# Kernel tuning notes

Measured on AMD Instinct MI355X. Metric: run time of the kernel, lower is better.

The kernel has to match this reference:

```python
import jax, jax.numpy as jnp
import numpy as np

S, H, HEADS = 2048, 1024, 16   # seq_len, hidden_size, num attention heads
E, NM, P = 256, 1024, 2048     # num entities, total mentions, num candidate pairs
PH = 1024                      # pair_hidden_size


def setup_inputs() -> dict:
    key = jax.random.key(0)
    ks = jax.random.split(key, 13)
    s = 1.0 / np.sqrt(H)
    return {
        "sequence_output": jax.random.normal(ks[0], (S, H), jnp.float32),
        "attention": jax.random.uniform(ks[1], (HEADS, S, S), jnp.float32),
        "mention_idx": jax.random.randint(ks[2], (NM,), 0, S, jnp.int32),
        "entity_ids": jnp.sort(jax.random.randint(ks[3], (NM,), 0, E, jnp.int32)),
        "pair_h": jax.random.randint(ks[4], (P,), 0, E, jnp.int32),
        "pair_t": jax.random.randint(ks[5], (P,), 0, E, jnp.int32),
        "W_head": jax.random.normal(ks[6], (H, PH), jnp.float32) * s,
        "b_head": jnp.zeros((PH,), jnp.float32),
        "W_tail": jax.random.normal(ks[7], (H, PH), jnp.float32) * s,
        "b_tail": jnp.zeros((PH,), jnp.float32),
        "W_ctx": jax.random.normal(ks[8], (H, PH), jnp.float32) * s,
        "W_bil": jax.random.normal(ks[9], (PH, PH), jnp.float32) * s,
        "b_bil": jnp.zeros((), jnp.float32),
    }


def reference(sequence_output, attention, mention_idx, entity_ids, pair_h, pair_t,
              W_head, b_head, W_tail, b_tail, W_ctx, W_bil, b_bil):
    # ---- entity aggregation: ragged segment logsumexp (embs) + segment mean (atts) ----
    vals = sequence_output[mention_idx]                               # [NM, H]
    counts = jax.ops.segment_sum(jnp.ones((NM,), vals.dtype), entity_ids, num_segments=E)
    has = counts > 0                                                  # [E]
    seg_max = jax.ops.segment_max(vals, entity_ids, num_segments=E)   # [E, H]
    seg_max = jnp.where(has[:, None], seg_max, 0.0)
    sums = jax.ops.segment_sum(jnp.exp(vals - seg_max[entity_ids]), entity_ids, num_segments=E)
    ent_emb = jnp.where(has[:, None],
                        seg_max + jnp.log(jnp.where(has[:, None], sums, 1.0)),
                        0.0)                                          # [E, H]
    m_att = jnp.transpose(attention[:, mention_idx, :], (1, 0, 2))    # [NM, HEADS, S]
    ent_att = jax.ops.segment_sum(m_att, entity_ids, num_segments=E)
    ent_att = ent_att / jnp.maximum(counts, 1.0)[:, None, None]       # [E, HEADS, S]

    # ---- pair scoring ----
    hs, ts = ent_emb[pair_h], ent_emb[pair_t]                         # [P, H]
    pair_att = (ent_att[pair_h] * ent_att[pair_t]).sum(axis=1)        # [P, S]
    pair_att = pair_att / (pair_att.sum(axis=-1, keepdims=True) + 1e-6)
    contexts = pair_att @ sequence_output                             # [P, H]
    ctx_p = contexts @ W_ctx                                          # [P, PH]
    z_s = jnp.tanh(hs @ W_head + b_head + ctx_p)
    z_o = jnp.tanh(ts @ W_tail + b_tail + ctx_p)
    logits = jnp.einsum('pi,ij,pj->p', z_s, W_bil, z_o) + b_bil       # [P]
    return logits
```

## Files before the change

### kernel.cpp

```cpp
#include <hip/hip_runtime.h>
#include <hip/hip_bf16.h>
#include <math.h>
#include <stdint.h>

#define S_LEN  2048
#define HID    1024
#define NHEADS 16
#define NE     256
#define NMEN   1024
#define NP     2048
#define PHID   1024

typedef __attribute__((ext_vector_type(8))) short bf16x8;
typedef __attribute__((ext_vector_type(4))) float f32x4;
typedef unsigned int uint;

__device__ inline void seg_bounds(const int* __restrict__ entity_ids, int e,
                                  int& start, int& end) {
    int lo = 0, hi = NMEN;
    while (lo < hi) { int mid = (lo + hi) >> 1; if (entity_ids[mid] < e) lo = mid + 1; else hi = mid; }
    start = lo;
    hi = NMEN;
    while (lo < hi) { int mid = (lo + hi) >> 1; if (entity_ids[mid] <= e) lo = mid + 1; else hi = mid; }
    end = lo;
}

__device__ __forceinline__ void load_lds16(const void* g, void* l) {
    __builtin_amdgcn_global_load_lds(
        (const __attribute__((address_space(1))) uint32_t*)g,
        (__attribute__((address_space(3))) uint32_t*)l,
        16, 0, 0);
}

__device__ __forceinline__ float bflo(uint u) { return __uint_as_float(u << 16); }
__device__ __forceinline__ float bfhi(uint u) { return __uint_as_float(u & 0xffff0000u); }
__device__ __forceinline__ uint pk2(float a, float b) {
    __hip_bfloat16 ha = __float2bfloat16(a), hb = __float2bfloat16(b);
    unsigned short ua = *(unsigned short*)&ha, ub = *(unsigned short*)&hb;
    return (uint)ua | ((uint)ub << 16);
}

__global__ void prep_ent_kernel(const float* __restrict__ seq,
                                const float* __restrict__ attention,
                                const float* __restrict__ w0, const float* __restrict__ w1,
                                const float* __restrict__ w2, const float* __restrict__ wbil,
                                const int* __restrict__ mention_idx,
                                const int* __restrict__ entity_ids,
                                __hip_bfloat16* __restrict__ seqB,
                                __hip_bfloat16* __restrict__ o0, __hip_bfloat16* __restrict__ o1,
                                __hip_bfloat16* __restrict__ o2, __hip_bfloat16* __restrict__ obil,
                                uint2* __restrict__ eaB,
                                __hip_bfloat16* __restrict__ ent_emb)
{
    __shared__ float tbuf[32][33];
    __shared__ int sb[2];
    int id = blockIdx.x;
    if (id < 1024) {
        long i = (long)id * 256 + threadIdx.x;
        const float4* in4 = (const float4*)seq;
        float4 a = in4[2 * i], b = in4[2 * i + 1];
        uint4 o;
        o.x = pk2(a.x, a.y); o.y = pk2(a.z, a.w);
        o.z = pk2(b.x, b.y); o.w = pk2(b.z, b.w);
        ((uint4*)seqB)[i] = o;
        return;
    }
    if (id < 4096) {
        int t = id - 1024;
        int z = t >> 10;
        const float* in = (z == 0) ? w0 : (z == 1) ? w1 : w2;
        __hip_bfloat16* out = (z == 0) ? o0 : (z == 1) ? o1 : o2;
        int r0 = ((t >> 5) & 31) * 32, c0 = (t & 31) * 32;
        int j = threadIdx.x & 31, i0 = threadIdx.x >> 5;
        for (int i = i0; i < 32; i += 8)
            tbuf[i][j] = in[(long)(r0 + i) * 1024 + c0 + j];
        __syncthreads();
        for (int i = i0; i < 32; i += 8)
            out[(long)(c0 + i) * 1024 + r0 + j] = __float2bfloat16(tbuf[j][i]);
        return;
    }
    if (id < 4608) {
        long i = (long)(id - 4096) * 256 + threadIdx.x;
        const float4* in4 = (const float4*)wbil;
        float4 a = in4[2 * i], b = in4[2 * i + 1];
        uint4 o;
        o.x = pk2(a.x, a.y); o.y = pk2(a.z, a.w);
        o.z = pk2(b.x, b.y); o.w = pk2(b.z, b.w);
        ((uint4*)obil)[i] = o;
        return;
    }
    int t = id - 4608;
    int e = t & 255, role = t >> 8;
    if (threadIdx.x == 0) { int s, tt; seg_bounds(entity_ids, e, s, tt); sb[0] = s; sb[1] = tt; }
    __syncthreads();
    int start = sb[0], end = sb[1];

    if (role < 16) {
        const float4* att4 = (const float4*)attention;
        int h = role;
        float inv = 1.f / fmaxf((float)(end - start), 1.f);
        for (int s4 = threadIdx.x; s4 < S_LEN / 4; s4 += 256) {
            float ax = 0.f, ay = 0.f, az = 0.f, aw = 0.f;
            for (int i = start; i < end; ++i) {
                float4 v = att4[((long)h * S_LEN + mention_idx[i]) * (S_LEN / 4) + s4];
                ax += v.x; ay += v.y; az += v.z; aw += v.w;
            }
            uint2 o; o.x = pk2(ax * inv, ay * inv); o.y = pk2(az * inv, aw * inv);
            eaB[((long)e * NHEADS + h) * (S_LEN / 4) + s4] = o;
        }
    } else {
        const float4* seq4 = (const float4*)seq;
        int col4 = threadIdx.x;
        uint2 o;
        if (end <= start) {
            o.x = 0; o.y = 0;
            ((uint2*)ent_emb)[(long)e * 256 + col4] = o;
            return;
        }
        float mx = -INFINITY, my = -INFINITY, mz = -INFINITY, mw = -INFINITY;
        for (int i = start; i < end; ++i) {
            float4 v = seq4[(long)mention_idx[i] * 256 + col4];
            mx = fmaxf(mx, v.x); my = fmaxf(my, v.y); mz = fmaxf(mz, v.z); mw = fmaxf(mw, v.w);
        }
        float sx = 0.f, sy = 0.f, sz = 0.f, sw = 0.f;
        for (int i = start; i < end; ++i) {
            float4 v = seq4[(long)mention_idx[i] * 256 + col4];
            sx += expf(v.x - mx); sy += expf(v.y - my); sz += expf(v.z - mz); sw += expf(v.w - mw);
        }
        o.x = pk2(mx + logf(sx), my + logf(sy));
        o.y = pk2(mz + logf(sz), mw + logf(sw));
        ((uint2*)ent_emb)[(long)e * 256 + col4] = o;
    }
}

template <int MODE>
__device__ __forceinline__ void gemm_epilogue(
    f32x4 (&acc)[4][4], void* __restrict__ Cout,
    const __hip_bfloat16* __restrict__ zvec, float* __restrict__ out,
    int M, int N, int bm, int bn, int bz, int wr, int wc, int lane)
{
    int lr = lane & 15;
    int q4 = (lane >> 4) * 4;
    if (MODE == 0) {
#pragma unroll
        for (int fm = 0; fm < 4; ++fm)
#pragma unroll
            for (int fn = 0; fn < 4; ++fn) {
                int row = bm + wr * 64 + fm * 16 + q4;
                int col = bn + wc * 64 + fn * 16 + lr;
#pragma unroll
                for (int r = 0; r < 4; ++r)
                    ((float*)Cout)[((long)bz * M + row + r) * N + col] = acc[fm][fn][r];
            }
    } else if (MODE == 1) {
#pragma unroll
        for (int fm = 0; fm < 4; ++fm)
#pragma unroll
            for (int fn = 0; fn < 4; ++fn) {
                int row = bm + wr * 64 + fm * 16 + q4;
                int col = bn + wc * 64 + fn * 16 + lr;
#pragma unroll
                for (int r = 0; r < 4; ++r)
                    ((__hip_bfloat16*)Cout)[(long)(row + r) * N + col] = __float2bfloat16(acc[fm][fn][r]);
            }
    } else if (MODE == 3) {
#pragma unroll
        for (int fm = 0; fm < 4; ++fm)
#pragma unroll
            for (int fn = 0; fn < 4; ++fn) {
                int row = bm + wr * 64 + fm * 16 + q4;
                int col = bn + wc * 64 + fn * 16 + lr;
#pragma unroll
                for (int r = 0; r < 4; ++r)
                    ((__hip_bfloat16*)Cout)[((long)bz * M + row + r) * N + col] = __float2bfloat16(acc[fm][fn][r]);
            }
    } else {
#pragma unroll
        for (int fm = 0; fm < 4; ++fm) {
#pragma unroll
            for (int r = 0; r < 4; ++r) {
                int row = bm + wr * 64 + fm * 16 + q4 + r;
                float v = 0.f;
#pragma unroll
                for (int fn = 0; fn < 4; ++fn) {
                    int col = bn + wc * 64 + fn * 16 + lr;
                    v += acc[fm][fn][r] * __bfloat162float(zvec[(long)row * N + col]);
                }
                v += __shfl_xor(v, 1, 64);
                v += __shfl_xor(v, 2, 64);
                v += __shfl_xor(v, 4, 64);
                v += __shfl_xor(v, 8, 64);
                if (lr == 0) atomicAdd(out + row, v);
            }
        }
    }
}

template <int MODE>
__device__ __forceinline__ void gemm_core(
    const __hip_bfloat16* __restrict__ A,
    const __hip_bfloat16* __restrict__ Bt,
    void* __restrict__ Cout, const __hip_bfloat16* __restrict__ zvec, float* __restrict__ out,
    int M, int N, int Kstride, int kLen,
    int bx, int by, int bz,
    short (*As)[128][8], short (*Bs)[128][8])
{
    int tid = threadIdx.x;
    int lane = tid & 63, wid = tid >> 6;
    int wr = wid >> 1, wc = wid & 1;
    int bm = by * 128, bn = bx * 128;
    int kBeg = bz * kLen;

    const __hip_bfloat16* gsrc[8];
    void* ldst[8];
#pragma unroll
    for (int i = 0; i < 8; ++i) {
        int c = wid * 8 + i;
        int isA = (c < 16) ? 1 : 0;
        int cc = isA ? c : c - 16;
        int kg2 = cc >> 1, rh = cc & 1;
        gsrc[i] = (isA ? A + (long)(bm + rh * 64 + lane) * Kstride
                       : Bt + (long)(bn + rh * 64 + lane) * Kstride) + kBeg + kg2 * 8;
        ldst[i] = isA ? (void*)&As[kg2][rh * 64][0] : (void*)&Bs[kg2][rh * 64][0];
    }

    f32x4 acc[4][4] = {};
    int kg = lane >> 4, lr = lane & 15;

    for (int k0 = 0; k0 < kLen; k0 += 64) {
#pragma unroll
        for (int i = 0; i < 8; ++i)
            load_lds16(gsrc[i] + k0, ldst[i]);
        __syncthreads();
#pragma unroll
        for (int sub = 0; sub < 2; ++sub) {
            bf16x8 af[4], bfr[4];
#pragma unroll
            for (int f = 0; f < 4; ++f) {
                af[f]  = *(const bf16x8*)&As[sub * 4 + kg][wr * 64 + f * 16 + lr][0];
                bfr[f] = *(const bf16x8*)&Bs[sub * 4 + kg][wc * 64 + f * 16 + lr][0];
            }
#pragma unroll
            for (int fm = 0; fm < 4; ++fm)
#pragma unroll
                for (int fn = 0; fn < 4; ++fn)
                    acc[fm][fn] = __builtin_amdgcn_mfma_f32_16x16x32_bf16(af[fm], bfr[fn], acc[fm][fn], 0, 0, 0);
        }
        __syncthreads();
    }
    gemm_epilogue<MODE>(acc, Cout, zvec, out, M, N, bm, bn, bz, wr, wc, lane);
}

template <int MODE>
__device__ __forceinline__ void gemm_core_db(
    const __hip_bfloat16* __restrict__ A,
    const __hip_bfloat16* __restrict__ Bt,
    void* __restrict__ Cout, const __hip_bfloat16* __restrict__ zvec, float* __restrict__ out,
    int M, int N, int Kstride, int kLen,
    int bx, int by, int bz,
    short (*As)[8][128][8], short (*Bs)[8][128][8])
{
    int tid = threadIdx.x;
    int lane = tid & 63, wid = tid >> 6;
    int wr = wid >> 1, wc = wid & 1;
    int bm = by * 128, bn = bx * 128;
    int kBeg = bz * kLen;

    const __hip_bfloat16* gsrc[8];
    void *ld0[8], *ld1[8];
#pragma unroll
    for (int i = 0; i < 8; ++i) {
        int c = wid * 8 + i;
        int isA = (c < 16) ? 1 : 0;
        int cc = isA ? c : c - 16;
        int kg2 = cc >> 1, rh = cc & 1;
        gsrc[i] = (isA ? A + (long)(bm + rh * 64 + lane) * Kstride
                       : Bt + (long)(bn + rh * 64 + lane) * Kstride) + kBeg + kg2 * 8;
        ld0[i] = isA ? (void*)&As[0][kg2][rh * 64][0] : (void*)&Bs[0][kg2][rh * 64][0];
        ld1[i] = isA ? (void*)&As[1][kg2][rh * 64][0] : (void*)&Bs[1][kg2][rh * 64][0];
    }

    f32x4 acc[4][4] = {};
    int kg = lane >> 4, lr = lane & 15;
    int nSteps = kLen >> 6;

#define STAGE_DB(t, ld) { _Pragma("unroll") \
    for (int i = 0; i < 8; ++i) load_lds16(gsrc[i] + (t) * 64, ld[i]); }
#define COMPUTE_DB(AsB, BsB) { _Pragma("unroll") \
    for (int sub = 0; sub < 2; ++sub) { \
        bf16x8 af[4], bfr[4]; \
        _Pragma("unroll") for (int f = 0; f < 4; ++f) { \
            af[f]  = *(const bf16x8*)&AsB[sub * 4 + kg][wr * 64 + f * 16 + lr][0]; \
            bfr[f] = *(const bf16x8*)&BsB[sub * 4 + kg][wc * 64 + f * 16 + lr][0]; \
        } \
        _Pragma("unroll") for (int fm = 0; fm < 4; ++fm) \
        _Pragma("unroll") for (int fn = 0; fn < 4; ++fn) \
            acc[fm][fn] = __builtin_amdgcn_mfma_f32_16x16x32_bf16(af[fm], bfr[fn], acc[fm][fn], 0, 0, 0); \
    } }

    STAGE_DB(0, ld0);
    __syncthreads();
    for (int step = 0; step < nSteps; step += 2) {
        STAGE_DB(step + 1, ld1);
        COMPUTE_DB(As[0], Bs[0]);
        __syncthreads();
        if (step + 2 < nSteps) STAGE_DB(step + 2, ld0);
        COMPUTE_DB(As[1], Bs[1]);
        __syncthreads();
    }
#undef STAGE_DB
#undef COMPUTE_DB
    gemm_epilogue<MODE>(acc, Cout, zvec, out, M, N, bm, bn, bz, wr, wc, lane);
}

__launch_bounds__(256)
__global__ void pair_seqw_ehet(const __hip_bfloat16* __restrict__ WctxT,
                               const __hip_bfloat16* __restrict__ seqB,
                               __hip_bfloat16* __restrict__ seqWT,
                               const __hip_bfloat16* __restrict__ embB,
                               const __hip_bfloat16* __restrict__ WhtT,
                               float* __restrict__ ehetP,
                               const uint4* __restrict__ ea,
                               const int* __restrict__ pair_h,
                               const int* __restrict__ pair_t,
                               uint4* __restrict__ patt)
{
    __shared__ short As[8][128][8];
    __shared__ short Bs[8][128][8];
    int id = blockIdx.x;
    if (id < 128) {
        gemm_core<1>(WctxT, seqB, seqWT, nullptr, nullptr,
                     PHID, S_LEN, HID, HID, id & 15, id >> 4, 0, As, Bs);
        return;
    }
    if (id < 256) {
        int u = id - 128;
        gemm_core<0>(embB, WhtT, ehetP, nullptr, nullptr,
                     NE, 2 * PHID, HID, HID / 4, u & 15, (u >> 4) & 1, u >> 5, As, Bs);
        return;
    }
    __shared__ float wsum[4];
    int p = id - 256;
    long bh = (long)pair_h[p] * NHEADS * (S_LEN / 8);
    long bt = (long)pair_t[p] * NHEADS * (S_LEN / 8);
    int s8 = threadIdx.x;
    float a0 = 0, a1 = 0, a2 = 0, a3 = 0, a4 = 0, a5 = 0, a6 = 0, a7 = 0;
#pragma unroll
    for (int h = 0; h < NHEADS; ++h) {
        uint4 xa = ea[bh + h * (S_LEN / 8) + s8];
        uint4 xb = ea[bt + h * (S_LEN / 8) + s8];
        a0 += bflo(xa.x) * bflo(xb.x); a1 += bfhi(xa.x) * bfhi(xb.x);
        a2 += bflo(xa.y) * bflo(xb.y); a3 += bfhi(xa.y) * bfhi(xb.y);
        a4 += bflo(xa.z) * bflo(xb.z); a5 += bfhi(xa.z) * bfhi(xb.z);
        a6 += bflo(xa.w) * bflo(xb.w); a7 += bfhi(xa.w) * bfhi(xb.w);
    }
    float psum = a0 + a1 + a2 + a3 + a4 + a5 + a6 + a7;
#pragma unroll
    for (int off = 32; off > 0; off >>= 1)
        psum += __shfl_down(psum, off, 64);
    int lane = threadIdx.x & 63, wid = threadIdx.x >> 6;
    if (lane == 0) wsum[wid] = psum;
    __syncthreads();
    float inv = 1.f / (wsum[0] + wsum[1] + wsum[2] + wsum[3] + 1e-6f);
    uint4 o;
    o.x = pk2(a0 * inv, a1 * inv); o.y = pk2(a2 * inv, a3 * inv);
    o.z = pk2(a4 * inv, a5 * inv); o.w = pk2(a6 * inv, a7 * inv);
    patt[(long)p * (S_LEN / 8) + s8] = o;
}

__launch_bounds__(256)
__global__ void gemm_ctxp_reduce(const __hip_bfloat16* __restrict__ pattB,
                                 const __hip_bfloat16* __restrict__ seqWT,
                                 __hip_bfloat16* __restrict__ ctxpB,
                                 const float* __restrict__ ehetP,
                                 float* __restrict__ ehet)
{
    __shared__ short As[2][8][128][8];
    __shared__ short Bs[2][8][128][8];
    int id = blockIdx.x;
    if (id < 512) {
        int f = (id & 7) * 64 + (id >> 3);
        int bx = f >> 6, inner = f & 63;
        int by = inner & 15, bz = inner >> 4;
        gemm_core_db<3>(pattB, seqWT, ctxpB, nullptr, nullptr,
                        NP, PHID, S_LEN, S_LEN / 4, bx, by, bz, As, Bs);
        return;
    }
    long i = (long)(id - 512) * 2048 + (long)threadIdx.x * 8;
    const long n = (long)NE * 2 * PHID;
    float4 s0 = make_float4(0.f, 0.f, 0.f, 0.f), s1 = s0;
#pragma unroll
    for (int s = 0; s < 4; ++s) {
        float4 a = *(const float4*)&ehetP[s * n + i];
        float4 b = *(const float4*)&ehetP[s * n + i + 4];
        s0.x += a.x; s0.y += a.y; s0.z += a.z; s0.w += a.w;
        s1.x += b.x; s1.y += b.y; s1.z += b.z; s1.w += b.w;
    }
    *(float4*)&ehet[i] = s0;
    *(float4*)&ehet[i + 4] = s1;
}

__global__ void zs_zo_kernel(const __hip_bfloat16* __restrict__ ctxpB,
                             const float* __restrict__ ehet,
                             const float* __restrict__ b_head,
                             const float* __restrict__ b_tail,
                             const int* __restrict__ pair_h,
                             const int* __restrict__ pair_t,
                             __hip_bfloat16* __restrict__ zs,
                             __hip_bfloat16* __restrict__ zo,
                             const float* __restrict__ b_bil, float* __restrict__ out)
{
    long base = ((long)blockIdx.x * 256 + threadIdx.x) * 4;
    if (base < NP) {
        float bb = b_bil[0];
#pragma unroll
        for (int i = 0; i < 4; ++i) out[base + i] = bb;
    }
    int p = (int)(base >> 10);
    int j = (int)(base & (PHID - 1));
    const long n = (long)NP * PHID;
    float c0 = 0.f, c1 = 0.f, c2 = 0.f, c3 = 0.f;
#pragma unroll
    for (int s = 0; s < 4; ++s) {
        uint2 u = *(const uint2*)&ctxpB[s * n + base];
        c0 += bflo(u.x); c1 += bfhi(u.x); c2 += bflo(u.y); c3 += bfhi(u.y);
    }
    float4 eh = *(const float4*)&ehet[(long)pair_h[p] * 2048 + j];
    float4 et = *(const float4*)&ehet[(long)pair_t[p] * 2048 + 1024 + j];
    float4 bh = *(const float4*)&b_head[j];
    float4 bt = *(const float4*)&b_tail[j];
    float h0 = tanhf(eh.x + bh.x + c0), h1 = tanhf(eh.y + bh.y + c1);
    float h2 = tanhf(eh.z + bh.z + c2), h3 = tanhf(eh.w + bh.w + c3);
    float t0 = tanhf(et.x + bt.x + c0), t1 = tanhf(et.y + bt.y + c1);
    float t2 = tanhf(et.z + bt.z + c2), t3 = tanhf(et.w + bt.w + c3);
    uint2 ozs; ozs.x = pk2(h0, h1); ozs.y = pk2(h2, h3);
    uint2 ozo; ozo.x = pk2(t0, t1); ozo.y = pk2(t2, t3);
    *(uint2*)&zs[base] = ozs;
    *(uint2*)&zo[base] = ozo;
}

template <int MODE>
__launch_bounds__(256)
__global__ void gemm_single_db(const __hip_bfloat16* __restrict__ A,
                               const __hip_bfloat16* __restrict__ Bt,
                               void* __restrict__ Cout,
                               const __hip_bfloat16* __restrict__ zvec,
                               float* __restrict__ out,
                               int M, int N, int Kstride, int kLen)
{
    __shared__ short As[2][8][128][8];
    __shared__ short Bs[2][8][128][8];
    gemm_core_db<MODE>(A, Bt, Cout, zvec, out, M, N, Kstride, kLen,
                       blockIdx.x, blockIdx.y, blockIdx.z, As, Bs);
}

extern "C" void kernel_launch(void* const* d_in, const int* in_sizes, int n_in,
                              void* d_out, int out_size, void* d_ws, size_t ws_size,
                              hipStream_t stream)
{
    const float* seq        = (const float*)d_in[0];
    const float* attention  = (const float*)d_in[1];
    const int*   mention_idx= (const int*)  d_in[2];
    const int*   entity_ids = (const int*)  d_in[3];
    const int*   pair_h     = (const int*)  d_in[4];
    const int*   pair_t     = (const int*)  d_in[5];
    const float* W_head     = (const float*)d_in[6];
    const float* b_head     = (const float*)d_in[7];
    const float* W_tail     = (const float*)d_in[8];
    const float* b_tail     = (const float*)d_in[9];
    const float* W_ctx      = (const float*)d_in[10];
    const float* W_bil      = (const float*)d_in[11];
    const float* b_bil      = (const float*)d_in[12];
    float* out = (float*)d_out;

    char* w = (char*)d_ws;
    __hip_bfloat16* seqB  = (__hip_bfloat16*)(w + 0);
    __hip_bfloat16* WctxT = (__hip_bfloat16*)(w + (4l << 20));
    __hip_bfloat16* WhtT  = (__hip_bfloat16*)(w + (6l << 20));
    __hip_bfloat16* WbilB = (__hip_bfloat16*)(w + (10l << 20));
    __hip_bfloat16* embB  = (__hip_bfloat16*)(w + (12l << 20));
    __hip_bfloat16* eaB   = (__hip_bfloat16*)(w + (13l << 20));
    __hip_bfloat16* pattB = (__hip_bfloat16*)(w + (29l << 20));
    __hip_bfloat16* seqWT = (__hip_bfloat16*)(w + (37l << 20));
    __hip_bfloat16* zsB   = (__hip_bfloat16*)(w + (41l << 20));
    __hip_bfloat16* zoB   = (__hip_bfloat16*)(w + (45l << 20));
    __hip_bfloat16* ctxpB = (__hip_bfloat16*)(w + (49l << 20));
    float* ehetP = (float*)(w + (65l << 20));
    float* ehet  = (float*)(w + (73l << 20));

    prep_ent_kernel<<<8960, 256, 0, stream>>>(seq, attention, W_ctx, W_head, W_tail, W_bil,
                                              mention_idx, entity_ids,
                                              seqB, WctxT, WhtT, WhtT + (long)PHID * HID, WbilB,
                                              (uint2*)eaB, embB);

    pair_seqw_ehet<<<2304, 256, 0, stream>>>(WctxT, seqB, seqWT, embB, WhtT, ehetP,
                                             (const uint4*)eaB, pair_h, pair_t, (uint4*)pattB);

    gemm_ctxp_reduce<<<768, 256, 0, stream>>>(pattB, seqWT, ctxpB, ehetP, ehet);

    zs_zo_kernel<<<2048, 256, 0, stream>>>(ctxpB, ehet, b_head, b_tail, pair_h, pair_t,
                                           zsB, zoB, b_bil, out);

    gemm_single_db<2><<<dim3(8, 16, 4), 256, 0, stream>>>(zoB, WbilB, nullptr, zsB, out,
                                                          NP, PHID, HID, HID / 4);
}
```

Measured before the change: 136.6 us.

## Reschedule stages: fuse seq bf16 cast into GEMM, move attention aggregation later

Drops the separate seq fp32-to-bf16 conversion pass. The seq×Wctx GEMM now loads fp32 B tiles directly and converts them to bf16 on the fly while filling LDS. The attention-mean aggregation moves from the first kernel into the second, running concurrently with the small GEMMs. The ehet partial reduction moves into the pair-attention kernel so the ctxp GEMM runs alone. The goal is better load balance across the launch sequence and less workspace traffic, at the cost of a non-async fp32 load path in one GEMM.

```diff
diff --git a/kernel.cpp b/kernel.cpp
--- a/kernel.cpp
+++ b/kernel.cpp
@@ -40,37 +40,24 @@
     return (uint)ua | ((uint)ub << 16);
 }
 
-__global__ void prep_ent_kernel(const float* __restrict__ seq,
-                                const float* __restrict__ attention,
-                                const float* __restrict__ w0, const float* __restrict__ w1,
-                                const float* __restrict__ w2, const float* __restrict__ wbil,
-                                const int* __restrict__ mention_idx,
-                                const int* __restrict__ entity_ids,
-                                __hip_bfloat16* __restrict__ seqB,
-                                __hip_bfloat16* __restrict__ o0, __hip_bfloat16* __restrict__ o1,
-                                __hip_bfloat16* __restrict__ o2, __hip_bfloat16* __restrict__ obil,
-                                uint2* __restrict__ eaB,
-                                __hip_bfloat16* __restrict__ ent_emb)
+__global__ void l0_kernel(const float* __restrict__ seq,
+                          const float* __restrict__ w0, const float* __restrict__ w1,
+                          const float* __restrict__ w2, const float* __restrict__ wbil,
+                          const int* __restrict__ mention_idx,
+                          const int* __restrict__ entity_ids,
+                          __hip_bfloat16* __restrict__ o0, __hip_bfloat16* __restrict__ o1,
+                          __hip_bfloat16* __restrict__ o2, __hip_bfloat16* __restrict__ obil,
+                          __hip_bfloat16* __restrict__ ent_emb)
 {
     __shared__ float tbuf[32][33];
     __shared__ int sb[2];
     int id = blockIdx.x;
-    if (id < 1024) {
-        long i = (long)id * 256 + threadIdx.x;
-        const float4* in4 = (const float4*)seq;
-        float4 a = in4[2 * i], b = in4[2 * i + 1];
-        uint4 o;
-        o.x = pk2(a.x, a.y); o.y = pk2(a.z, a.w);
-        o.z = pk2(b.x, b.y); o.w = pk2(b.z, b.w);
-        ((uint4*)seqB)[i] = o;
-        return;
-    }
-    if (id < 4096) {
-        int t = id - 1024;
-        int z = t >> 10;
+    if (id < 3072) {
+        int z = id >> 10;
         const float* in = (z == 0) ? w0 : (z == 1) ? w1 : w2;
         __hip_bfloat16* out = (z == 0) ? o0 : (z == 1) ? o1 : o2;
-        int r0 = ((t >> 5) & 31) * 32, c0 = (t & 31) * 32;
+        int t = id & 1023;
+        int r0 = (t >> 5) * 32, c0 = (t & 31) * 32;
         int j = threadIdx.x & 31, i0 = threadIdx.x >> 5;
         for (int i = i0; i < 32; i += 8)
             tbuf[i][j] = in[(long)(r0 + i) * 1024 + c0 + j];
@@ -79,8 +66,8 @@
             out[(long)(c0 + i) * 1024 + r0 + j] = __float2bfloat16(tbuf[j][i]);
         return;
     }
-    if (id < 4608) {
-        long i = (long)(id - 4096) * 256 + threadIdx.x;
+    if (id < 3584) {
+        long i = (long)(id - 3072) * 256 + threadIdx.x;
         const float4* in4 = (const float4*)wbil;
         float4 a = in4[2 * i], b = in4[2 * i + 1];
         uint4 o;
@@ -89,48 +76,31 @@
         ((uint4*)obil)[i] = o;
         return;
     }
-    int t = id - 4608;
-    int e = t & 255, role = t >> 8;
+    int e = id - 3584;
     if (threadIdx.x == 0) { int s, tt; seg_bounds(entity_ids, e, s, tt); sb[0] = s; sb[1] = tt; }
     __syncthreads();
     int start = sb[0], end = sb[1];
-
-    if (role < 16) {
-        const float4* att4 = (const float4*)attention;
-        int h = role;
-        float inv = 1.f / fmaxf((float)(end - start), 1.f);
-        for (int s4 = threadIdx.x; s4 < S_LEN / 4; s4 += 256) {
-            float ax = 0.f, ay = 0.f, az = 0.f, aw = 0.f;
-            for (int i = start; i < end; ++i) {
-                float4 v = att4[((long)h * S_LEN + mention_idx[i]) * (S_LEN / 4) + s4];
-                ax += v.x; ay += v.y; az += v.z; aw += v.w;
-            }
-            uint2 o; o.x = pk2(ax * inv, ay * inv); o.y = pk2(az * inv, aw * inv);
-            eaB[((long)e * NHEADS + h) * (S_LEN / 4) + s4] = o;
-        }
-    } else {
-        const float4* seq4 = (const float4*)seq;
-        int col4 = threadIdx.x;
-        uint2 o;
-        if (end <= start) {
-            o.x = 0; o.y = 0;
-            ((uint2*)ent_emb)[(long)e * 256 + col4] = o;
-            return;
-        }
-        float mx = -INFINITY, my = -INFINITY, mz = -INFINITY, mw = -INFINITY;
-        for (int i = start; i < end; ++i) {
-            float4 v = seq4[(long)mention_idx[i] * 256 + col4];
-            mx = fmaxf(mx, v.x); my = fmaxf(my, v.y); mz = fmaxf(mz, v.z); mw = fmaxf(mw, v.w);
-        }
-        float sx = 0.f, sy = 0.f, sz = 0.f, sw = 0.f;
-        for (int i = start; i < end; ++i) {
-            float4 v = seq4[(long)mention_idx[i] * 256 + col4];
-            sx += expf(v.x - mx); sy += expf(v.y - my); sz += expf(v.z - mz); sw += expf(v.w - mw);
-        }
-        o.x = pk2(mx + logf(sx), my + logf(sy));
-        o.y = pk2(mz + logf(sz), mw + logf(sw));
+    const float4* seq4 = (const float4*)seq;
+    int col4 = threadIdx.x;
+    uint2 o;
+    if (end <= start) {
+        o.x = 0; o.y = 0;
         ((uint2*)ent_emb)[(long)e * 256 + col4] = o;
-    }
+        return;
+    }
+    float mx = -INFINITY, my = -INFINITY, mz = -INFINITY, mw = -INFINITY;
+    for (int i = start; i < end; ++i) {
+        float4 v = seq4[(long)mention_idx[i] * 256 + col4];
+        mx = fmaxf(mx, v.x); my = fmaxf(my, v.y); mz = fmaxf(mz, v.z); mw = fmaxf(mw, v.w);
+    }
+    float sx = 0.f, sy = 0.f, sz = 0.f, sw = 0.f;
+    for (int i = start; i < end; ++i) {
+        float4 v = seq4[(long)mention_idx[i] * 256 + col4];
+        sx += expf(v.x - mx); sy += expf(v.y - my); sz += expf(v.z - mz); sw += expf(v.w - mw);
+    }
+    o.x = pk2(mx + logf(sx), my + logf(sy));
+    o.y = pk2(mz + logf(sz), mw + logf(sw));
+    ((uint2*)ent_emb)[(long)e * 256 + col4] = o;
 }
 
 template <int MODE>
@@ -196,97 +166,7 @@
     }
 }
 
-template <int MODE>
-__device__ __forceinline__ void gemm_core(
-    const __hip_bfloat16* __restrict__ A,
-    const __hip_bfloat16* __restrict__ Bt,
-    void* __restrict__ Cout, const __hip_bfloat16* __restrict__ zvec, float* __restrict__ out,
-    int M, int N, int Kstride, int kLen,
-    int bx, int by, int bz,
-    short (*As)[128][8], short (*Bs)[128][8])
-{
-    int tid = threadIdx.x;
-    int lane = tid & 63, wid = tid >> 6;
-    int wr = wid >> 1, wc = wid & 1;
-    int bm = by * 128, bn = bx * 128;
-    int kBeg = bz * kLen;
-
-    const __hip_bfloat16* gsrc[8];
-    void* ldst[8];
-#pragma unroll
-    for (int i = 0; i < 8; ++i) {
-        int c = wid * 8 + i;
-        int isA = (c < 16) ? 1 : 0;
-        int cc = isA ? c : c - 16;
-        int kg2 = cc >> 1, rh = cc & 1;
-        gsrc[i] = (isA ? A + (long)(bm + rh * 64 + lane) * Kstride
-                       : Bt + (long)(bn + rh * 64 + lane) * Kstride) + kBeg + kg2 * 8;
-        ldst[i] = isA ? (void*)&As[kg2][rh * 64][0] : (void*)&Bs[kg2][rh * 64][0];
-    }
-
-    f32x4 acc[4][4] = {};
-    int kg = lane >> 4, lr = lane & 15;
-
-    for (int k0 = 0; k0 < kLen; k0 += 64) {
-#pragma unroll
-        for (int i = 0; i < 8; ++i)
-            load_lds16(gsrc[i] + k0, ldst[i]);
-        __syncthreads();
-#pragma unroll
-        for (int sub = 0; sub < 2; ++sub) {
-            bf16x8 af[4], bfr[4];
-#pragma unroll
-            for (int f = 0; f < 4; ++f) {
-                af[f]  = *(const bf16x8*)&As[sub * 4 + kg][wr * 64 + f * 16 + lr][0];
-                bfr[f] = *(const bf16x8*)&Bs[sub * 4 + kg][wc * 64 + f * 16 + lr][0];
-            }
-#pragma unroll
-            for (int fm = 0; fm < 4; ++fm)
-#pragma unroll
-                for (int fn = 0; fn < 4; ++fn)
-                    acc[fm][fn] = __builtin_amdgcn_mfma_f32_16x16x32_bf16(af[fm], bfr[fn], acc[fm][fn], 0, 0, 0);
-        }
-        __syncthreads();
-    }
-    gemm_epilogue<MODE>(acc, Cout, zvec, out, M, N, bm, bn, bz, wr, wc, lane);
-}
-
-template <int MODE>
-__device__ __forceinline__ void gemm_core_db(
-    const __hip_bfloat16* __restrict__ A,
-    const __hip_bfloat16* __restrict__ Bt,
-    void* __restrict__ Cout, const __hip_bfloat16* __restrict__ zvec, float* __restrict__ out,
-    int M, int N, int Kstride, int kLen,
-    int bx, int by, int bz,
-    short (*As)[8][128][8], short (*Bs)[8][128][8])
-{
-    int tid = threadIdx.x;
-    int lane = tid & 63, wid = tid >> 6;
-    int wr = wid >> 1, wc = wid & 1;
-    int bm = by * 128, bn = bx * 128;
-    int kBeg = bz * kLen;
-
-    const __hip_bfloat16* gsrc[8];
-    void *ld0[8], *ld1[8];
-#pragma unroll
-    for (int i = 0; i < 8; ++i) {
-        int c = wid * 8 + i;
-        int isA = (c < 16) ? 1 : 0;
-        int cc = isA ? c : c - 16;
-        int kg2 = cc >> 1, rh = cc & 1;
-        gsrc[i] = (isA ? A + (long)(bm + rh * 64 + lane) * Kstride
-                       : Bt + (long)(bn + rh * 64 + lane) * Kstride) + kBeg + kg2 * 8;
-        ld0[i] = isA ? (void*)&As[0][kg2][rh * 64][0] : (void*)&Bs[0][kg2][rh * 64][0];
-        ld1[i] = isA ? (void*)&As[1][kg2][rh * 64][0] : (void*)&Bs[1][kg2][rh * 64][0];
-    }
-
-    f32x4 acc[4][4] = {};
-    int kg = lane >> 4, lr = lane & 15;
-    int nSteps = kLen >> 6;
-
-#define STAGE_DB(t, ld) { _Pragma("unroll") \
-    for (int i = 0; i < 8; ++i) load_lds16(gsrc[i] + (t) * 64, ld[i]); }
-#define COMPUTE_DB(AsB, BsB) { _Pragma("unroll") \
+#define COMPUTE_TILE(AsB, BsB) { _Pragma("unroll") \
     for (int sub = 0; sub < 2; ++sub) { \
         bf16x8 af[4], bfr[4]; \
         _Pragma("unroll") for (int f = 0; f < 4; ++f) { \
@@ -298,39 +178,177 @@
             acc[fm][fn] = __builtin_amdgcn_mfma_f32_16x16x32_bf16(af[fm], bfr[fn], acc[fm][fn], 0, 0, 0); \
     } }
 
+template <int MODE>
+__device__ __forceinline__ void gemm_core(
+    const __hip_bfloat16* __restrict__ A,
+    const __hip_bfloat16* __restrict__ Bt,
+    void* __restrict__ Cout, const __hip_bfloat16* __restrict__ zvec, float* __restrict__ out,
+    int M, int N, int Kstride, int kLen,
+    int bx, int by, int bz,
+    short (*As)[128][8], short (*Bs)[128][8])
+{
+    int tid = threadIdx.x;
+    int lane = tid & 63, wid = tid >> 6;
+    int wr = wid >> 1, wc = wid & 1;
+    int bm = by * 128, bn = bx * 128;
+    int kBeg = bz * kLen;
+
+    const __hip_bfloat16* gsrc[8];
+    void* ldst[8];
+#pragma unroll
+    for (int i = 0; i < 8; ++i) {
+        int c = wid * 8 + i;
+        int isA = (c < 16) ? 1 : 0;
+        int cc = isA ? c : c - 16;
+        int kg2 = cc >> 1, rh = cc & 1;
+        gsrc[i] = (isA ? A + (long)(bm + rh * 64 + lane) * Kstride
+                       : Bt + (long)(bn + rh * 64 + lane) * Kstride) + kBeg + kg2 * 8;
+        ldst[i] = isA ? (void*)&As[kg2][rh * 64][0] : (void*)&Bs[kg2][rh * 64][0];
+    }
+
+    f32x4 acc[4][4] = {};
+    int kg = lane >> 4, lr = lane & 15;
+
+    for (int k0 = 0; k0 < kLen; k0 += 64) {
+#pragma unroll
+        for (int i = 0; i < 8; ++i)
+            load_lds16(gsrc[i] + k0, ldst[i]);
+        __syncthreads();
+        COMPUTE_TILE(As, Bs);
+        __syncthreads();
+    }
+    gemm_epilogue<MODE>(acc, Cout, zvec, out, M, N, bm, bn, bz, wr, wc, lane);
+}
+
+__device__ __forceinline__ void gemm_core_f32b(
+    const __hip_bfloat16* __restrict__ A,
+    const float* __restrict__ Bf,
+    __hip_bfloat16* __restrict__ Cout,
+    int M, int N, int Kstride, int kLen,
+    int bx, int by,
+    short (*As)[128][8], short (*Bs)[128][8])
+{
+    int tid = threadIdx.x;
+    int lane = tid & 63, wid = tid >> 6;
+    int wr = wid >> 1, wc = wid & 1;
+    int bm = by * 128, bn = bx * 128;
+
+    const __hip_bfloat16* gA[8];
+    const float* gB[8];
+    void* ldA[8];
+    void* ldB[8];
+#pragma unroll
+    for (int i = 0; i < 8; ++i) {
+        int c = wid * 8 + i;
+        if (c < 16) {
+            int kg2 = c >> 1, rh = c & 1;
+            gA[i] = A + (long)(bm + rh * 64 + lane) * Kstride + kg2 * 8;
+            ldA[i] = (void*)&As[kg2][rh * 64][0];
+            gB[i] = nullptr; ldB[i] = nullptr;
+        } else {
+            int cc = c - 16;
+            int kg2 = cc >> 1, rh = cc & 1;
+            gB[i] = Bf + (long)(bn + rh * 64 + lane) * Kstride + kg2 * 8;
+            ldB[i] = (void*)&Bs[kg2][rh * 64 + lane][0];
+            gA[i] = nullptr; ldA[i] = nullptr;
+        }
+    }
+
+    f32x4 acc[4][4] = {};
+    int kg = lane >> 4, lr = lane & 15;
+
+    for (int k0 = 0; k0 < kLen; k0 += 64) {
+        if (wid < 2) {
+#pragma unroll
+            for (int i = 0; i < 8; ++i)
+                load_lds16(gA[i] + k0, ldA[i]);
+        } else {
+#pragma unroll
+            for (int i = 0; i < 8; ++i) {
+                const float* p = gB[i] + k0;
+                float4 x = *(const float4*)p;
+                float4 y = *(const float4*)(p + 4);
+                uint4 v;
+                v.x = pk2(x.x, x.y); v.y = pk2(x.z, x.w);
+                v.z = pk2(y.x, y.y); v.w = pk2(y.z, y.w);
+                *(uint4*)ldB[i] = v;
+            }
+        }
+        __syncthreads();
+        COMPUTE_TILE(As, Bs);
+        __syncthreads();
+    }
+    gemm_epilogue<1>(acc, (void*)Cout, nullptr, nullptr, M, N, bm, bn, 0, wr, wc, lane);
+}
+
+template <int MODE>
+__device__ __forceinline__ void gemm_core_db(
+    const __hip_bfloat16* __restrict__ A,
+    const __hip_bfloat16* __restrict__ Bt,
+    void* __restrict__ Cout, const __hip_bfloat16* __restrict__ zvec, float* __restrict__ out,
+    int M, int N, int Kstride, int kLen,
+    int bx, int by, int bz,
+    short (*As)[8][128][8], short (*Bs)[8][128][8])
+{
+    int tid = threadIdx.x;
+    int lane = tid & 63, wid = tid >> 6;
+    int wr = wid >> 1, wc = wid & 1;
+    int bm = by * 128, bn = bx * 128;
+    int kBeg = bz * kLen;
+
+    const __hip_bfloat16* gsrc[8];
+    void *ld0[8], *ld1[8];
+#pragma unroll
+    for (int i = 0; i < 8; ++i) {
+        int c = wid * 8 + i;
+        int isA = (c < 16) ? 1 : 0;
+        int cc = isA ? c : c - 16;
+        int kg2 = cc >> 1, rh = cc & 1;
+        gsrc[i] = (isA ? A + (long)(bm + rh * 64 + lane) * Kstride
+                       : Bt + (long)(bn + rh * 64 + lane) * Kstride) + kBeg + kg2 * 8;
+        ld0[i] = isA ? (void*)&As[0][kg2][rh * 64][0] : (void*)&Bs[0][kg2][rh * 64][0];
+        ld1[i] = isA ? (void*)&As[1][kg2][rh * 64][0] : (void*)&Bs[1][kg2][rh * 64][0];
+    }
+
+    f32x4 acc[4][4] = {};
+    int kg = lane >> 4, lr = lane & 15;
+    int nSteps = kLen >> 6;
+
+#define STAGE_DB(t, ld) { _Pragma("unroll") \
+    for (int i = 0; i < 8; ++i) load_lds16(gsrc[i] + (t) * 64, ld[i]); }
+
     STAGE_DB(0, ld0);
     __syncthreads();
     for (int step = 0; step < nSteps; step += 2) {
         STAGE_DB(step + 1, ld1);
-        COMPUTE_DB(As[0], Bs[0]);
+        COMPUTE_TILE(As[0], Bs[0]);
         __syncthreads();
         if (step + 2 < nSteps) STAGE_DB(step + 2, ld0);
-        COMPUTE_DB(As[1], Bs[1]);
+        COMPUTE_TILE(As[1], Bs[1]);
         __syncthreads();
     }
 #undef STAGE_DB
-#undef COMPUTE_DB
     gemm_epilogue<MODE>(acc, Cout, zvec, out, M, N, bm, bn, bz, wr, wc, lane);
 }
 
 __launch_bounds__(256)
-__global__ void pair_seqw_ehet(const __hip_bfloat16* __restrict__ WctxT,
-                               const __hip_bfloat16* __restrict__ seqB,
-                               __hip_bfloat16* __restrict__ seqWT,
-                               const __hip_bfloat16* __restrict__ embB,
-                               const __hip_bfloat16* __restrict__ WhtT,
-                               float* __restrict__ ehetP,
-                               const uint4* __restrict__ ea,
-                               const int* __restrict__ pair_h,
-                               const int* __restrict__ pair_t,
-                               uint4* __restrict__ patt)
+__global__ void l1_kernel(const __hip_bfloat16* __restrict__ WctxT,
+                          const float* __restrict__ seq,
+                          __hip_bfloat16* __restrict__ seqWT,
+                          const __hip_bfloat16* __restrict__ embB,
+                          const __hip_bfloat16* __restrict__ WhtT,
+                          float* __restrict__ ehetP,
+                          const float* __restrict__ attention,
+                          const int* __restrict__ mention_idx,
+                          const int* __restrict__ entity_ids,
+                          uint2* __restrict__ eaB)
 {
     __shared__ short As[8][128][8];
     __shared__ short Bs[8][128][8];
+    __shared__ int sb[2];
     int id = blockIdx.x;
     if (id < 128) {
-        gemm_core<1>(WctxT, seqB, seqWT, nullptr, nullptr,
-                     PHID, S_LEN, HID, HID, id & 15, id >> 4, 0, As, Bs);
+        gemm_core_f32b(WctxT, seq, seqWT, PHID, S_LEN, HID, HID, id & 15, id >> 4, As, Bs);
         return;
     }
     if (id < 256) {
@@ -339,7 +357,48 @@
                      NE, 2 * PHID, HID, HID / 4, u & 15, (u >> 4) & 1, u >> 5, As, Bs);
         return;
     }
+    int t = id - 256;
+    int e = t & 255, h = t >> 8;
+    if (threadIdx.x == 0) { int s, tt; seg_bounds(entity_ids, e, s, tt); sb[0] = s; sb[1] = tt; }
+    __syncthreads();
+    int start = sb[0], end = sb[1];
+    const float4* att4 = (const float4*)attention;
+    float inv = 1.f / fmaxf((float)(end - start), 1.f);
+    for (int s4 = threadIdx.x; s4 < S_LEN / 4; s4 += 256) {
+        float ax = 0.f, ay = 0.f, az = 0.f, aw = 0.f;
+        for (int i = start; i < end; ++i) {
+            float4 v = att4[((long)h * S_LEN + mention_idx[i]) * (S_LEN / 4) + s4];
+            ax += v.x; ay += v.y; az += v.z; aw += v.w;
+        }
+        uint2 o; o.x = pk2(ax * inv, ay * inv); o.y = pk2(az * inv, aw * inv);
+        eaB[((long)e * NHEADS + h) * (S_LEN / 4) + s4] = o;
+    }
+}
+
+__global__ void l2_kernel(const float* __restrict__ ehetP,
+                          float* __restrict__ ehet,
+                          const uint4* __restrict__ ea,
+                          const int* __restrict__ pair_h,
+                          const int* __restrict__ pair_t,
+                          uint4* __restrict__ patt)
+{
     __shared__ float wsum[4];
+    int id = blockIdx.x;
+    if (id < 256) {
+        long i = (long)id * 2048 + (long)threadIdx.x * 8;
+        const long n = (long)NE * 2 * PHID;
+        float4 s0 = make_float4(0.f, 0.f, 0.f, 0.f), s1 = s0;
+#pragma unroll
+        for (int s = 0; s < 4; ++s) {
+            float4 a = *(const float4*)&ehetP[s * n + i];
+            float4 b = *(const float4*)&ehetP[s * n + i + 4];
+            s0.x += a.x; s0.y += a.y; s0.z += a.z; s0.w += a.w;
+            s1.x += b.x; s1.y += b.y; s1.z += b.z; s1.w += b.w;
+        }
+        *(float4*)&ehet[i] = s0;
+        *(float4*)&ehet[i + 4] = s1;
+        return;
+    }
     int p = id - 256;
     long bh = (long)pair_h[p] * NHEADS * (S_LEN / 8);
     long bt = (long)pair_t[p] * NHEADS * (S_LEN / 8);
@@ -369,35 +428,18 @@
 }
 
 __launch_bounds__(256)
-__global__ void gemm_ctxp_reduce(const __hip_bfloat16* __restrict__ pattB,
-                                 const __hip_bfloat16* __restrict__ seqWT,
-                                 __hip_bfloat16* __restrict__ ctxpB,
-                                 const float* __restrict__ ehetP,
-                                 float* __restrict__ ehet)
+__global__ void gemm_ctxp(const __hip_bfloat16* __restrict__ pattB,
+                          const __hip_bfloat16* __restrict__ seqWT,
+                          __hip_bfloat16* __restrict__ ctxpB)
 {
     __shared__ short As[2][8][128][8];
     __shared__ short Bs[2][8][128][8];
     int id = blockIdx.x;
-    if (id < 512) {
-        int f = (id & 7) * 64 + (id >> 3);
-        int bx = f >> 6, inner = f & 63;
-        int by = inner & 15, bz = inner >> 4;
-        gemm_core_db<3>(pattB, seqWT, ctxpB, nullptr, nullptr,
-                        NP, PHID, S_LEN, S_LEN / 4, bx, by, bz, As, Bs);
-        return;
-    }
-    long i = (long)(id - 512) * 2048 + (long)threadIdx.x * 8;
-    const long n = (long)NE * 2 * PHID;
-    float4 s0 = make_float4(0.f, 0.f, 0.f, 0.f), s1 = s0;
-#pragma unroll
-    for (int s = 0; s < 4; ++s) {
-        float4 a = *(const float4*)&ehetP[s * n + i];
-        float4 b = *(const float4*)&ehetP[s * n + i + 4];
-        s0.x += a.x; s0.y += a.y; s0.z += a.z; s0.w += a.w;
-        s1.x += b.x; s1.y += b.y; s1.z += b.z; s1.w += b.w;
-    }
-    *(float4*)&ehet[i] = s0;
-    *(float4*)&ehet[i + 4] = s1;
+    int f = (id & 7) * 64 + (id >> 3);
+    int bx = f >> 6, inner = f & 63;
+    int by = inner & 15, bz = inner >> 4;
+    gemm_core_db<3>(pattB, seqWT, ctxpB, nullptr, nullptr,
+                    NP, PHID, S_LEN, S_LEN / 4, bx, by, bz, As, Bs);
 }
 
 __global__ void zs_zo_kernel(const __hip_bfloat16* __restrict__ ctxpB,
@@ -474,29 +516,30 @@
     float* out = (float*)d_out;
 
     char* w = (char*)d_ws;
-    __hip_bfloat16* seqB  = (__hip_bfloat16*)(w + 0);
-    __hip_bfloat16* WctxT = (__hip_bfloat16*)(w + (4l << 20));
-    __hip_bfloat16* WhtT  = (__hip_bfloat16*)(w + (6l << 20));
-    __hip_bfloat16* WbilB = (__hip_bfloat16*)(w + (10l << 20));
-    __hip_bfloat16* embB  = (__hip_bfloat16*)(w + (12l << 20));
-    __hip_bfloat16* eaB   = (__hip_bfloat16*)(w + (13l << 20));
-    __hip_bfloat16* pattB = (__hip_bfloat16*)(w + (29l << 20));
-    __hip_bfloat16* seqWT = (__hip_bfloat16*)(w + (37l << 20));
-    __hip_bfloat16* zsB   = (__hip_bfloat16*)(w + (41l << 20));
-    __hip_bfloat16* zoB   = (__hip_bfloat16*)(w + (45l << 20));
-    __hip_bfloat16* ctxpB = (__hip_bfloat16*)(w + (49l << 20));
-    float* ehetP = (float*)(w + (65l << 20));
-    float* ehet  = (float*)(w + (73l << 20));
-
-    prep_ent_kernel<<<8960, 256, 0, stream>>>(seq, attention, W_ctx, W_head, W_tail, W_bil,
-                                              mention_idx, entity_ids,
-                                              seqB, WctxT, WhtT, WhtT + (long)PHID * HID, WbilB,
-                                              (uint2*)eaB, embB);
-
-    pair_seqw_ehet<<<2304, 256, 0, stream>>>(WctxT, seqB, seqWT, embB, WhtT, ehetP,
-                                             (const uint4*)eaB, pair_h, pair_t, (uint4*)pattB);
-
-    gemm_ctxp_reduce<<<768, 256, 0, stream>>>(pattB, seqWT, ctxpB, ehetP, ehet);
+    __hip_bfloat16* WctxT = (__hip_bfloat16*)(w + 0);
+    __hip_bfloat16* WhtT  = (__hip_bfloat16*)(w + (2l << 20));
+    __hip_bfloat16* WbilB = (__hip_bfloat16*)(w + (6l << 20));
+    __hip_bfloat16* embB  = (__hip_bfloat16*)(w + (8l << 20));
+    __hip_bfloat16* eaB   = (__hip_bfloat16*)(w + (9l << 20));
+    __hip_bfloat16* pattB = (__hip_bfloat16*)(w + (25l << 20));
+    __hip_bfloat16* seqWT = (__hip_bfloat16*)(w + (33l << 20));
+    __hip_bfloat16* zsB   = (__hip_bfloat16*)(w + (37l << 20));
+    __hip_bfloat16* zoB   = (__hip_bfloat16*)(w + (41l << 20));
+    __hip_bfloat16* ctxpB = (__hip_bfloat16*)(w + (45l << 20));
+    float* ehetP = (float*)(w + (61l << 20));
+    float* ehet  = (float*)(w + (69l << 20));
+
+    l0_kernel<<<3840, 256, 0, stream>>>(seq, W_ctx, W_head, W_tail, W_bil,
+                                        mention_idx, entity_ids,
+                                        WctxT, WhtT, WhtT + (long)PHID * HID, WbilB, embB);
+
+    l1_kernel<<<4352, 256, 0, stream>>>(WctxT, seq, seqWT, embB, WhtT, ehetP,
+                                        attention, mention_idx, entity_ids, (uint2*)eaB);
+
+    l2_kernel<<<2304, 256, 0, stream>>>(ehetP, ehet, (const uint4*)eaB,
+                                        pair_h, pair_t, (uint4*)pattB);
+
+    gemm_ctxp<<<512, 256, 0, stream>>>(pattB, seqWT, ctxpB);
 
     zs_zo_kernel<<<2048, 256, 0, stream>>>(ctxpB, ehet, b_head, b_tail, pair_h, pair_t,
                                            zsB, zoB, b_bil, out);
```

Measured after the change: 164.1 us. 20.1% more time.
